# Performance work log

Measured on AMD Instinct MI355X. Metric: run time of the kernel, lower is better.

The kernel has to match this reference:

```python
import jax, jax.numpy as jnp
import numpy as np

DIM = 1024
HEADS = 16
DIM_HEAD = 64
INNER = HEADS * DIM_HEAD  # 1024
MLP = 4096


def setup_inputs() -> dict:
    key = jax.random.key(0)
    ks = jax.random.split(key, 10)
    s = lambda k, shape, fan: jax.random.normal(k, shape, jnp.float32) * (fan ** -0.5)
    return {
        "x": jax.random.normal(ks[0], (4, 2048, DIM), jnp.float32),
        "ln1_g": jnp.ones((DIM,), jnp.float32),
        "ln1_b": jnp.zeros((DIM,), jnp.float32),
        "w_qkv": s(ks[1], (DIM, 3 * INNER), DIM),
        "w_out": s(ks[2], (INNER, DIM), INNER),
        "b_out": jnp.zeros((DIM,), jnp.float32),
        "ln2_g": jnp.ones((DIM,), jnp.float32),
        "ln2_b": jnp.zeros((DIM,), jnp.float32),
        "w1": s(ks[3], (DIM, MLP), DIM),
        "b1": jnp.zeros((MLP,), jnp.float32),
        "w2": s(ks[4], (MLP, DIM), MLP),
        "b2": jnp.zeros((DIM,), jnp.float32),
    }


def layernorm(x, g, b, eps=1e-5):
    mu = jnp.mean(x, axis=-1, keepdims=True)
    var = jnp.mean(jnp.square(x - mu), axis=-1, keepdims=True)
    return (x - mu) * jax.lax.rsqrt(var + eps) * g + b


def reference(x, ln1_g, ln1_b, w_qkv, w_out, b_out, ln2_g, ln2_b, w1, b1, w2, b2):
    b, n, d = x.shape
    h, dh = HEADS, DIM_HEAD
    scale = dh ** -0.5

    # Attention sub-block (pre-LN)
    xn = layernorm(x, ln1_g, ln1_b)
    qkv = xn @ w_qkv                                   # [b, n, 3*inner]
    q, k, v = jnp.split(qkv, 3, axis=-1)
    to_heads = lambda t: t.reshape(b, n, h, dh).transpose(0, 2, 1, 3)  # [b,h,n,dh]
    q, k, v = to_heads(q), to_heads(k), to_heads(v)
    dots = jnp.einsum('bhqd,bhkd->bhqk', q, k) * scale  # [b,h,n,n]
    attn = jax.nn.softmax(dots, axis=-1)
    out = jnp.einsum('bhqk,bhkd->bhqd', attn, v)        # [b,h,n,dh]
    out = out.transpose(0, 2, 1, 3).reshape(b, n, h * dh)
    x = x + out @ w_out + b_out

    # MLP sub-block (pre-LN)
    xn = layernorm(x, ln2_g, ln2_b)
    hdn = jax.nn.gelu(xn @ w1 + b1, approximate=False)
    x = x + hdn @ w2 + b2
    return x
```

## Files before the change

kernel.cpp:

```cpp
#include <hip/hip_runtime.h>
#include <hip/hip_bf16.h>
#include <math.h>

#define DIM   1024
#define HEADS 16
#define DH    64
#define SEQ   2048
#define BATCH 4
#define ROWS  (BATCH * SEQ)
#define MLP   4096
#define QKV3  (3 * DIM)

typedef __bf16    bf16x8 __attribute__((ext_vector_type(8)));
typedef __bf16    bf16x4 __attribute__((ext_vector_type(4)));
typedef float     f32x4  __attribute__((ext_vector_type(4)));
typedef unsigned int u32x2 __attribute__((ext_vector_type(2)));

__device__ inline void store_out(float* p, float v)           { *p = v; }
__device__ inline void store_out(__hip_bfloat16* p, float v)  { *p = __float2bfloat16(v); }

#define GLP(p) ((const __attribute__((address_space(1))) void*)(p))
#define LDP(p) ((__attribute__((address_space(3))) void*)(p))

__device__ inline float fast_exp2(float x) {
#if __has_builtin(__builtin_amdgcn_exp2f)
    return __builtin_amdgcn_exp2f(x);
#else
    return __expf(x * 0.69314718056f);
#endif
}

__device__ inline float fast_rcp(float x) {
#if __has_builtin(__builtin_amdgcn_rcpf)
    return __builtin_amdgcn_rcpf(x);
#else
    return 1.f / x;
#endif
}

__global__ __launch_bounds__(256) void ln_kernel(
    const float* __restrict__ x,
    const float* __restrict__ g,
    const float* __restrict__ b,
    __hip_bfloat16* __restrict__ y)
{
    const int row = blockIdx.x;
    const int tid = threadIdx.x;
    __shared__ float red[256];

    const float* xr = x + (size_t)row * DIM;
    float vals[4];
    float s = 0.f;
#pragma unroll
    for (int i = 0; i < 4; ++i) {
        vals[i] = xr[tid + i * 256];
        s += vals[i];
    }
    red[tid] = s; __syncthreads();
    for (int t = 128; t > 0; t >>= 1) { if (tid < t) red[tid] += red[tid + t]; __syncthreads(); }
    const float mu = red[0] * (1.f / DIM);
    __syncthreads();

    float vs = 0.f;
#pragma unroll
    for (int i = 0; i < 4; ++i) { float d = vals[i] - mu; vs += d * d; }
    red[tid] = vs; __syncthreads();
    for (int t = 128; t > 0; t >>= 1) { if (tid < t) red[tid] += red[tid + t]; __syncthreads(); }
    const float rstd = rsqrtf(red[0] * (1.f / DIM) + 1e-5f);

#pragma unroll
    for (int i = 0; i < 4; ++i) {
        const int c = tid + i * 256;
        float o = (vals[i] - mu) * rstd * g[c] + b[c];
        y[(size_t)row * DIM + c] = __float2bfloat16(o);
    }
}

__global__ __launch_bounds__(256) void transpose_w_kernel(
    const float* __restrict__ B, __bf16* __restrict__ BT,
    int Nfull, int r0, int c0, int Ksub)
{
    const int kb = blockIdx.x, nb = blockIdx.y;
    __shared__ float T[32][33];
    const int t  = threadIdx.x;
    const int r  = t >> 3;
    const int cq = (t & 7) * 4;

    f32x4 v = *(const f32x4*)(B + (size_t)(r0 + kb * 32 + r) * Nfull + c0 + nb * 32 + cq);
    T[r][cq] = v[0]; T[r][cq + 1] = v[1]; T[r][cq + 2] = v[2]; T[r][cq + 3] = v[3];
    __syncthreads();

    bf16x4 o;
#pragma unroll
    for (int i = 0; i < 4; ++i) o[i] = (__bf16)T[cq + i][r];
    *(bf16x4*)(BT + (size_t)(nb * 32 + r) * Ksub + kb * 32 + cq) = o;
}

template <typename OutT>
__global__ __launch_bounds__(256) void gemm_bt_kernel(
    const __bf16* __restrict__ A,
    const __bf16* __restrict__ BT,
    const float* __restrict__ bias,
    const float* __restrict__ res,
    OutT* __restrict__ C,
    int M, int N, int K, int do_gelu)
{
    __shared__ __align__(16) __bf16 As[128 * 32];
    __shared__ __align__(16) __bf16 Bs[128 * 32];

    const int tid  = threadIdx.x;
    const int lane = tid & 63;
    const int w    = tid >> 6;
    const int q    = lane >> 4;
    const int c    = lane & 15;
    const int mw   = (w >> 1) * 64;
    const int nw   = (w & 1) * 64;

    const int rowTile = blockIdx.y * 128;
    const int colTile = blockIdx.x * 128;

    const int j0   = 2 * w;
    const int sR0  = j0 * 16 + (lane >> 2);
    const int sK   = (lane & 3) * 8;
    const __bf16* Ap0 = A  + (size_t)(rowTile + sR0) * K + sK;
    const __bf16* Ap1 = A  + (size_t)(rowTile + sR0 + 16) * K + sK;
    const __bf16* Bp0 = BT + (size_t)(colTile + sR0) * K + sK;
    const __bf16* Bp1 = BT + (size_t)(colTile + sR0 + 16) * K + sK;
    __bf16* AsD0 = &As[(j0    ) * 512];
    __bf16* AsD1 = &As[(j0 + 1) * 512];
    __bf16* BsD0 = &Bs[(j0    ) * 512];
    __bf16* BsD1 = &Bs[(j0 + 1) * 512];

    f32x4 acc[4][4];
#pragma unroll
    for (int i = 0; i < 4; ++i)
#pragma unroll
        for (int j = 0; j < 4; ++j) acc[i][j] = (f32x4){0.f, 0.f, 0.f, 0.f};

    for (int k0 = 0; k0 < K; k0 += 32) {
        __builtin_amdgcn_global_load_lds(GLP(Ap0 + k0), LDP(AsD0), 16, 0, 0);
        __builtin_amdgcn_global_load_lds(GLP(Ap1 + k0), LDP(AsD1), 16, 0, 0);
        __builtin_amdgcn_global_load_lds(GLP(Bp0 + k0), LDP(BsD0), 16, 0, 0);
        __builtin_amdgcn_global_load_lds(GLP(Bp1 + k0), LDP(BsD1), 16, 0, 0);
        __syncthreads();

        bf16x8 af[4], bf[4];
#pragma unroll
        for (int mt = 0; mt < 4; ++mt)
            af[mt] = *(const bf16x8*)(&As[(mw + mt * 16 + c) * 32 + q * 8]);
#pragma unroll
        for (int nt = 0; nt < 4; ++nt)
            bf[nt] = *(const bf16x8*)(&Bs[(nw + nt * 16 + c) * 32 + q * 8]);

#pragma unroll
        for (int mt = 0; mt < 4; ++mt)
#pragma unroll
            for (int nt = 0; nt < 4; ++nt)
                acc[mt][nt] = __builtin_amdgcn_mfma_f32_16x16x32_bf16(af[mt], bf[nt], acc[mt][nt], 0, 0, 0);
        __syncthreads();
    }

#pragma unroll
    for (int nt = 0; nt < 4; ++nt) {
        const int col = colTile + nw + nt * 16 + c;
        const float bv = bias ? bias[col] : 0.f;
#pragma unroll
        for (int mt = 0; mt < 4; ++mt) {
#pragma unroll
            for (int r = 0; r < 4; ++r) {
                const int row = rowTile + mw + mt * 16 + q * 4 + r;
                float v = acc[mt][nt][r] + bv;
                if (do_gelu) {
                    const float y2 = fminf(1.5957691216057308f * v * (1.f + 0.044715f * v * v), 80.f);
                    const float e  = __expf(y2);
                    v = v * e * fast_rcp(e + 1.f);
                }
                if (res) v += res[(size_t)row * N + col];
                store_out(&C[(size_t)row * N + col], v);
            }
        }
    }
}

#define KB  64
#define QB  256
#define KTP 72
#define VTP 72
#define NT  (SEQ / KB)
#define NEG_M0_LOG2E  (-11.541560327111707f)
#define QSCALE_LOG2E  (0.18033688011112043f)

__global__ __launch_bounds__(256, 2) void flash_attn_kernel(
    const __hip_bfloat16* __restrict__ qkv,
    __hip_bfloat16* __restrict__ out)
{
    const int tid  = threadIdx.x;
    const int w    = tid >> 6;
    const int lane = tid & 63;
    const int quad = lane >> 4;
    const int c    = lane & 15;

    const int h = blockIdx.y;
    const int b = blockIdx.z;
    const size_t base = (size_t)b * SEQ;
    const int qbase = blockIdx.x * QB + w * 64;

    __shared__ __align__(16) __bf16 Kt[KB * KTP];
    __shared__ __align__(16) __bf16 Vt[DH * VTP];

    const __bf16* qkvb = (const __bf16*)qkv;

    bf16x8 aq[4][2];
#pragma unroll
    for (int qg = 0; qg < 4; ++qg)
#pragma unroll
        for (int kk = 0; kk < 2; ++kk) {
            bf16x8 t = *(const bf16x8*)(qkvb + (base + qbase + qg * 16 + c) * QKV3
                                        + h * DH + kk * 32 + quad * 8);
#pragma unroll
            for (int j = 0; j < 8; ++j) aq[qg][kk][j] = (__bf16)(QSCALE_LOG2E * (float)t[j]);
        }

    bf16x8 onesv;
#pragma unroll
    for (int j = 0; j < 8; ++j) onesv[j] = (__bf16)1.0f;

    f32x4 o[4][4];
#pragma unroll
    for (int qg = 0; qg < 4; ++qg)
#pragma unroll
        for (int ch = 0; ch < 4; ++ch) o[qg][ch] = (f32x4){0.f, 0.f, 0.f, 0.f};
    f32x4 ol[4] = {{0,0,0,0},{0,0,0,0},{0,0,0,0},{0,0,0,0}};

    const int sR = tid >> 3;
    const int sD = (tid & 7) * 8;
    const __bf16* Kg = qkvb + (base + sR) * QKV3 + DIM + h * DH + sD;

    const int vm = tid & 7;
    const int d0 = (tid >> 3) * 2;
    const __bf16* Vg = qkvb + (base + 8 * vm) * QKV3 + 2 * DIM + h * DH + d0;
    const int bpos = 32 * (vm >> 2) + 16 * (vm & 1) + 4 * ((vm >> 1) & 1);

    bf16x8 kA, kB_;
    unsigned vv[8];
    kA  = *(const bf16x8*)(Kg);
    kB_ = *(const bf16x8*)(Kg + (size_t)32 * QKV3);
#pragma unroll
    for (int j = 0; j < 8; ++j)
        vv[j] = *(const unsigned*)(Vg + (size_t)j * QKV3);

    for (int kt = 0; kt < NT; ++kt) {
        *(bf16x8*)(&Kt[sR * KTP + sD])        = kA;
        *(bf16x8*)(&Kt[(sR + 32) * KTP + sD]) = kB_;
        {
            const unsigned lo01 = (vv[0] & 0xFFFFu) | (vv[1] << 16);
            const unsigned lo23 = (vv[2] & 0xFFFFu) | (vv[3] << 16);
            const unsigned lo45 = (vv[4] & 0xFFFFu) | (vv[5] << 16);
            const unsigned lo67 = (vv[6] & 0xFFFFu) | (vv[7] << 16);
            const unsigned hi01 = (vv[0] >> 16) | (vv[1] & 0xFFFF0000u);
            const unsigned hi23 = (vv[2] >> 16) | (vv[3] & 0xFFFF0000u);
            const unsigned hi45 = (vv[4] >> 16) | (vv[5] & 0xFFFF0000u);
            const unsigned hi67 = (vv[6] >> 16) | (vv[7] & 0xFFFF0000u);
            *(u32x2*)(&Vt[(d0    ) * VTP + bpos])     = (u32x2){lo01, lo23};
            *(u32x2*)(&Vt[(d0    ) * VTP + bpos + 8]) = (u32x2){lo45, lo67};
            *(u32x2*)(&Vt[(d0 + 1) * VTP + bpos])     = (u32x2){hi01, hi23};
            *(u32x2*)(&Vt[(d0 + 1) * VTP + bpos + 8]) = (u32x2){hi45, hi67};
        }
        __syncthreads();

        if (kt + 1 < NT) {
            const size_t koff = (size_t)(kt + 1) * KB * QKV3;
            kA  = *(const bf16x8*)(Kg + koff);
            kB_ = *(const bf16x8*)(Kg + koff + (size_t)32 * QKV3);
#pragma unroll
            for (int j = 0; j < 8; ++j)
                vv[j] = *(const unsigned*)(Vg + koff + (size_t)j * QKV3);
        }

        bf16x8 kf[4][2];
#pragma unroll
        for (int kg = 0; kg < 4; ++kg)
#pragma unroll
            for (int kk = 0; kk < 2; ++kk)
                kf[kg][kk] = *(const bf16x8*)(&Kt[(kg * 16 + c) * KTP + kk * 32 + quad * 8]);

        bf16x8 ap[4][2];
#pragma unroll
        for (int qg = 0; qg < 4; ++qg) {
            f32x4 st[4];
#pragma unroll
            for (int kg = 0; kg < 4; ++kg)
                st[kg] = (f32x4){NEG_M0_LOG2E, NEG_M0_LOG2E, NEG_M0_LOG2E, NEG_M0_LOG2E};
            __builtin_amdgcn_s_setprio(1);
#pragma unroll
            for (int kg = 0; kg < 4; ++kg)
#pragma unroll
                for (int kk = 0; kk < 2; ++kk)
                    st[kg] = __builtin_amdgcn_mfma_f32_16x16x32_bf16(kf[kg][kk], aq[qg][kk], st[kg], 0, 0, 0);
            __builtin_amdgcn_s_setprio(0);

#pragma unroll
            for (int kg = 0; kg < 4; ++kg)
#pragma unroll
                for (int r = 0; r < 4; ++r)
                    ap[qg][kg >> 1][(kg & 1) * 4 + r] = (__bf16)fast_exp2(st[kg][r]);
        }

        __builtin_amdgcn_s_setprio(1);
#pragma unroll
        for (int qg = 0; qg < 4; ++qg) {
            ol[qg] = __builtin_amdgcn_mfma_f32_16x16x32_bf16(ap[qg][0], onesv, ol[qg], 0, 0, 0);
            ol[qg] = __builtin_amdgcn_mfma_f32_16x16x32_bf16(ap[qg][1], onesv, ol[qg], 0, 0, 0);
        }
#pragma unroll
        for (int h2 = 0; h2 < 2; ++h2)
#pragma unroll
            for (int ch = 0; ch < 4; ++ch) {
                bf16x8 bv = *(const bf16x8*)(&Vt[(ch * 16 + c) * VTP + h2 * 32 + quad * 8]);
#pragma unroll
                for (int qg = 0; qg < 4; ++qg)
                    o[qg][ch] = __builtin_amdgcn_mfma_f32_16x16x32_bf16(ap[qg][h2], bv, o[qg][ch], 0, 0, 0);
            }
        __builtin_amdgcn_s_setprio(0);
        __syncthreads();
    }

#pragma unroll
    for (int qg = 0; qg < 4; ++qg) {
#pragma unroll
        for (int r = 0; r < 4; ++r) {
            const float inv = 1.f / ol[qg][r];
            const size_t row = base + qbase + qg * 16 + quad * 4 + r;
#pragma unroll
            for (int ch = 0; ch < 4; ++ch)
                out[row * DIM + h * DH + ch * 16 + c] = __float2bfloat16(o[qg][ch][r] * inv);
        }
    }
}

extern "C" void kernel_launch(void* const* d_in, const int* in_sizes, int n_in,
                              void* d_out, int out_size, void* d_ws, size_t ws_size,
                              hipStream_t stream)
{
    const float* x     = (const float*)d_in[0];
    const float* ln1_g = (const float*)d_in[1];
    const float* ln1_b = (const float*)d_in[2];
    const float* w_qkv = (const float*)d_in[3];
    const float* w_out = (const float*)d_in[4];
    const float* b_out = (const float*)d_in[5];
    const float* ln2_g = (const float*)d_in[6];
    const float* ln2_b = (const float*)d_in[7];
    const float* w1    = (const float*)d_in[8];
    const float* b1    = (const float*)d_in[9];
    const float* w2    = (const float*)d_in[10];
    const float* b2    = (const float*)d_in[11];
    float* out = (float*)d_out;

    char* ws = (char*)d_ws;
    const size_t MiB = 1024 * 1024;
    __hip_bfloat16* X   = (__hip_bfloat16*)(ws);
    __bf16*         wT  = (__bf16*)(ws + 16 * MiB);
    __hip_bfloat16* qkv = (__hip_bfloat16*)(ws + 24 * MiB);
    __bf16*         hdn = (__bf16*)(ws + 24 * MiB);

    dim3 blk(256);

    transpose_w_kernel<<<dim3(DIM / 32, QKV3 / 32), blk, 0, stream>>>(w_qkv, wT, QKV3, 0, 0, DIM);
    ln_kernel<<<dim3(ROWS), blk, 0, stream>>>(x, ln1_g, ln1_b, X);
    gemm_bt_kernel<__hip_bfloat16><<<dim3(QKV3 / 128, ROWS / 128), blk, 0, stream>>>(
        (const __bf16*)X, wT, nullptr, nullptr, qkv, ROWS, QKV3, DIM, 0);
    flash_attn_kernel<<<dim3(SEQ / QB, HEADS, BATCH), blk, 0, stream>>>(qkv, X);
    transpose_w_kernel<<<dim3(DIM / 32, DIM / 32), blk, 0, stream>>>(w_out, wT, DIM, 0, 0, DIM);
    gemm_bt_kernel<float><<<dim3(DIM / 128, ROWS / 128), blk, 0, stream>>>(
        (const __bf16*)X, wT, b_out, x, out, ROWS, DIM, DIM, 0);
    ln_kernel<<<dim3(ROWS), blk, 0, stream>>>(out, ln2_g, ln2_b, X);

    transpose_w_kernel<<<dim3(DIM / 32, 2048 / 32), blk, 0, stream>>>(w1, wT, MLP, 0, 0, DIM);
    gemm_bt_kernel<__hip_bfloat16><<<dim3(2048 / 128, ROWS / 128), blk, 0, stream>>>(
        (const __bf16*)X, wT, b1, nullptr, (__hip_bfloat16*)hdn, ROWS, 2048, DIM, 1);
    transpose_w_kernel<<<dim3(2048 / 32, DIM / 32), blk, 0, stream>>>(w2, wT, DIM, 0, 0, 2048);
    gemm_bt_kernel<float><<<dim3(DIM / 128, ROWS / 128), blk, 0, stream>>>(
        hdn, wT, b2, out, out, ROWS, DIM, 2048, 0);

    transpose_w_kernel<<<dim3(DIM / 32, 2048 / 32), blk, 0, stream>>>(w1, wT, MLP, 0, 2048, DIM);
    gemm_bt_kernel<__hip_bfloat16><<<dim3(2048 / 128, ROWS / 128), blk, 0, stream>>>(
        (const __bf16*)X, wT, b1 + 2048, nullptr, (__hip_bfloat16*)hdn, ROWS, 2048, DIM, 1);
    transpose_w_kernel<<<dim3(2048 / 32, DIM / 32), blk, 0, stream>>>(w2, wT, DIM, 2048, 0, 2048);
    gemm_bt_kernel<float><<<dim3(DIM / 128, ROWS / 128), blk, 0, stream>>>(
        hdn, wT, nullptr, out, out, ROWS, DIM, 2048, 0);
}
```

Baseline: 644.6 us.

## Double-buffer LDS in GEMM and enlarge tiles to 256x128 with 512 threads

Measured after the change: 602.2 us. 6.6% less time.

```diff
diff --git a/kernel.cpp b/kernel.cpp
--- a/kernel.cpp
+++ b/kernel.cpp
@@ -97,7 +97,7 @@
 }
 
 template <typename OutT>
-__global__ __launch_bounds__(256) void gemm_bt_kernel(
+__global__ __launch_bounds__(512, 3) void gemm_bt_kernel(
     const __bf16* __restrict__ A,
     const __bf16* __restrict__ BT,
     const float* __restrict__ bias,
@@ -105,8 +105,8 @@
     OutT* __restrict__ C,
     int M, int N, int K, int do_gelu)
 {
-    __shared__ __align__(16) __bf16 As[128 * 32];
-    __shared__ __align__(16) __bf16 Bs[128 * 32];
+    __shared__ __align__(16) __bf16 As[2][256 * 32];
+    __shared__ __align__(16) __bf16 Bs[2][128 * 32];
 
     const int tid  = threadIdx.x;
     const int lane = tid & 63;
@@ -116,20 +116,15 @@
     const int mw   = (w >> 1) * 64;
     const int nw   = (w & 1) * 64;
 
-    const int rowTile = blockIdx.y * 128;
+    const int rowTile = blockIdx.y * 256;
     const int colTile = blockIdx.x * 128;
 
-    const int j0   = 2 * w;
-    const int sR0  = j0 * 16 + (lane >> 2);
-    const int sK   = (lane & 3) * 8;
-    const __bf16* Ap0 = A  + (size_t)(rowTile + sR0) * K + sK;
-    const __bf16* Ap1 = A  + (size_t)(rowTile + sR0 + 16) * K + sK;
-    const __bf16* Bp0 = BT + (size_t)(colTile + sR0) * K + sK;
-    const __bf16* Bp1 = BT + (size_t)(colTile + sR0 + 16) * K + sK;
-    __bf16* AsD0 = &As[(j0    ) * 512];
-    __bf16* AsD1 = &As[(j0 + 1) * 512];
-    __bf16* BsD0 = &Bs[(j0    ) * 512];
-    __bf16* BsD1 = &Bs[(j0 + 1) * 512];
+    const int sRow = tid >> 2;
+    const int sK   = (tid & 3) * 8;
+    const __bf16* Ap0 = A  + (size_t)(rowTile + sRow) * K + sK;
+    const __bf16* Ap1 = A  + (size_t)(rowTile + 128 + sRow) * K + sK;
+    const __bf16* Bp  = BT + (size_t)(colTile + sRow) * K + sK;
+    const int wd = w * 512;
 
     f32x4 acc[4][4];
 #pragma unroll
@@ -137,26 +132,34 @@
 #pragma unroll
         for (int j = 0; j < 4; ++j) acc[i][j] = (f32x4){0.f, 0.f, 0.f, 0.f};
 
+    __builtin_amdgcn_global_load_lds(GLP(Ap0), LDP(&As[0][wd]),        16, 0, 0);
+    __builtin_amdgcn_global_load_lds(GLP(Ap1), LDP(&As[0][4096 + wd]), 16, 0, 0);
+    __builtin_amdgcn_global_load_lds(GLP(Bp ), LDP(&Bs[0][wd]),        16, 0, 0);
+    __syncthreads();
+
     for (int k0 = 0; k0 < K; k0 += 32) {
-        __builtin_amdgcn_global_load_lds(GLP(Ap0 + k0), LDP(AsD0), 16, 0, 0);
-        __builtin_amdgcn_global_load_lds(GLP(Ap1 + k0), LDP(AsD1), 16, 0, 0);
-        __builtin_amdgcn_global_load_lds(GLP(Bp0 + k0), LDP(BsD0), 16, 0, 0);
-        __builtin_amdgcn_global_load_lds(GLP(Bp1 + k0), LDP(BsD1), 16, 0, 0);
-        __syncthreads();
+        const int cur = (k0 >> 5) & 1;
+        if (k0 + 32 < K) {
+            const int nxt = cur ^ 1;
+            __builtin_amdgcn_global_load_lds(GLP(Ap0 + k0 + 32), LDP(&As[nxt][wd]),        16, 0, 0);
+            __builtin_amdgcn_global_load_lds(GLP(Ap1 + k0 + 32), LDP(&As[nxt][4096 + wd]), 16, 0, 0);
+            __builtin_amdgcn_global_load_lds(GLP(Bp  + k0 + 32), LDP(&Bs[nxt][wd]),        16, 0, 0);
+        }
 
         bf16x8 af[4], bf[4];
 #pragma unroll
         for (int mt = 0; mt < 4; ++mt)
-            af[mt] = *(const bf16x8*)(&As[(mw + mt * 16 + c) * 32 + q * 8]);
+            af[mt] = *(const bf16x8*)(&As[cur][(mw + mt * 16 + c) * 32 + q * 8]);
 #pragma unroll
         for (int nt = 0; nt < 4; ++nt)
-            bf[nt] = *(const bf16x8*)(&Bs[(nw + nt * 16 + c) * 32 + q * 8]);
+            bf[nt] = *(const bf16x8*)(&Bs[cur][(nw + nt * 16 + c) * 32 + q * 8]);
 
 #pragma unroll
         for (int mt = 0; mt < 4; ++mt)
 #pragma unroll
             for (int nt = 0; nt < 4; ++nt)
                 acc[mt][nt] = __builtin_amdgcn_mfma_f32_16x16x32_bf16(af[mt], bf[nt], acc[mt][nt], 0, 0, 0);
+
         __syncthreads();
     }
 
@@ -364,28 +367,29 @@
     __bf16*         hdn = (__bf16*)(ws + 24 * MiB);
 
     dim3 blk(256);
+    dim3 blk512(512);
 
     transpose_w_kernel<<<dim3(DIM / 32, QKV3 / 32), blk, 0, stream>>>(w_qkv, wT, QKV3, 0, 0, DIM);
     ln_kernel<<<dim3(ROWS), blk, 0, stream>>>(x, ln1_g, ln1_b, X);
-    gemm_bt_kernel<__hip_bfloat16><<<dim3(QKV3 / 128, ROWS / 128), blk, 0, stream>>>(
+    gemm_bt_kernel<__hip_bfloat16><<<dim3(QKV3 / 128, ROWS / 256), blk512, 0, stream>>>(
         (const __bf16*)X, wT, nullptr, nullptr, qkv, ROWS, QKV3, DIM, 0);
     flash_attn_kernel<<<dim3(SEQ / QB, HEADS, BATCH), blk, 0, stream>>>(qkv, X);
     transpose_w_kernel<<<dim3(DIM / 32, DIM / 32), blk, 0, stream>>>(w_out, wT, DIM, 0, 0, DIM);
-    gemm_bt_kernel<float><<<dim3(DIM / 128, ROWS / 128), blk, 0, stream>>>(
+    gemm_bt_kernel<float><<<dim3(DIM / 128, ROWS / 256), blk512, 0, stream>>>(
         (const __bf16*)X, wT, b_out, x, out, ROWS, DIM, DIM, 0);
     ln_kernel<<<dim3(ROWS), blk, 0, stream>>>(out, ln2_g, ln2_b, X);
 
     transpose_w_kernel<<<dim3(DIM / 32, 2048 / 32), blk, 0, stream>>>(w1, wT, MLP, 0, 0, DIM);
-    gemm_bt_kernel<__hip_bfloat16><<<dim3(2048 / 128, ROWS / 128), blk, 0, stream>>>(
+    gemm_bt_kernel<__hip_bfloat16><<<dim3(2048 / 128, ROWS / 256), blk512, 0, stream>>>(
         (const __bf16*)X, wT, b1, nullptr, (__hip_bfloat16*)hdn, ROWS, 2048, DIM, 1);
     transpose_w_kernel<<<dim3(2048 / 32, DIM / 32), blk, 0, stream>>>(w2, wT, DIM, 0, 0, 2048);
-    gemm_bt_kernel<float><<<dim3(DIM / 128, ROWS / 128), blk, 0, stream>>>(
+    gemm_bt_kernel<float><<<dim3(DIM / 128, ROWS / 256), blk512, 0, stream>>>(
         hdn, wT, b2, out, out, ROWS, DIM, 2048, 0);
 
     transpose_w_kernel<<<dim3(DIM / 32, 2048 / 32), blk, 0, stream>>>(w1, wT, MLP, 0, 2048, DIM);
-    gemm_bt_kernel<__hip_bfloat16><<<dim3(2048 / 128, ROWS / 128), blk, 0, stream>>>(
+    gemm_bt_kernel<__hip_bfloat16><<<dim3(2048 / 128, ROWS / 256), blk512, 0, stream>>>(
         (const __bf16*)X, wT, b1 + 2048, nullptr, (__hip_bfloat16*)hdn, ROWS, 2048, DIM, 1);
     transpose_w_kernel<<<dim3(2048 / 32, DIM / 32), blk, 0, stream>>>(w2, wT, DIM, 2048, 0, 2048);
-    gemm_bt_kernel<float><<<dim3(DIM / 128, ROWS / 128), blk, 0, stream>>>(
+    gemm_bt_kernel<float><<<dim3(DIM / 128, ROWS / 256), blk512, 0, stream>>>(
         hdn, wT, nullptr, out, out, ROWS, DIM, 2048, 0);
 }
```
